# Kernel tuning notes

Measured on AMD Instinct MI355X. Metric: run time of the kernel, lower is better.

## Reference

```python
import jax, jax.numpy as jnp
import numpy as np
import math

N_HEADS = 64
N_KV_HEADS = 8
HEAD_DIM = 128
DIM = 8192
SEQLEN = 2048
KVLEN = 2048
BSZ = 1


def setup_inputs() -> dict:
    key = jax.random.key(0)
    k1, k2, k3, k4, k5 = jax.random.split(key, 5)
    xq = jax.random.normal(k1, (SEQLEN, N_HEADS, BSZ, HEAD_DIM), dtype=jnp.float32)
    keys = jax.random.normal(k2, (BSZ, N_KV_HEADS, KVLEN, HEAD_DIM), dtype=jnp.float32)
    values = jax.random.normal(k3, (BSZ, N_KV_HEADS, KVLEN, HEAD_DIM), dtype=jnp.float32)
    attn_mask = jax.random.normal(k4, (SEQLEN, 1, 1, KVLEN), dtype=jnp.float32)
    wo_w = jax.random.normal(k5, (DIM, DIM), dtype=jnp.float32) * (1.0 / math.sqrt(DIM))
    return {"xq": xq, "keys": keys, "values": values, "attn_mask": attn_mask, "wo_w": wo_w}


def reference(xq, keys, values, attn_mask, wo_w):
    n_rep = N_HEADS // N_KV_HEADS
    bsz = xq.shape[2]
    seqlen = xq.shape[0]
    # repeat_kv: expand kv heads to n_heads (torch expand+reshape == jnp.repeat on head axis)
    k = jnp.repeat(keys, n_rep, axis=1)    # (b, n_heads, kv, d)
    v = jnp.repeat(values, n_rep, axis=1)  # (b, n_heads, kv, d)
    q = jnp.transpose(xq, (2, 1, 0, 3))    # (b, n_heads, s, d)
    mask = jnp.transpose(attn_mask, (2, 1, 0, 3))  # (b_or_1, h_or_1, s, kv)
    scores = jnp.einsum('bhsd,bhtd->bhst', q, k) / math.sqrt(HEAD_DIM)
    scores = scores + mask
    probs = jax.nn.softmax(scores.astype(jnp.float32), axis=-1).astype(q.dtype)
    out = jnp.einsum('bhst,bhtd->bhsd', probs, v)  # (b, h, s, d)
    out = jnp.transpose(out, (0, 2, 1, 3)).reshape(bsz, seqlen, -1)  # (b, s, h*d)
    return out @ wo_w.T  # Linear wo, no bias
```

## Files before the change

### kernel.cpp

```cpp
#include <hip/hip_runtime.h>
#include <hip/hip_bf16.h>
#include <stdint.h>


typedef __bf16 bf16;
typedef __attribute__((ext_vector_type(8))) __bf16 bf16x8;
typedef __attribute__((ext_vector_type(4))) __bf16 bf16x4;
typedef __attribute__((ext_vector_type(4))) float f32x4;
typedef __attribute__((ext_vector_type(16))) float f32x16;
typedef __attribute__((ext_vector_type(4))) unsigned int u32x4;

#define N_HEADS 64
#define N_KVH   8
#define HDIM    128
#define SEQ     2048
#define KVL     2048
#define DIM     8192

__device__ __forceinline__ void gload16(const void* g, void* l) {
  __builtin_amdgcn_global_load_lds((const __attribute__((address_space(1))) void*)g,
                                   (__attribute__((address_space(3))) void*)l,
                                   16, 0, 0);
}

__device__ __forceinline__ unsigned pack2(float lo, float hi) {
  union { bf16 h; unsigned short u; } a, b;
  a.h = (bf16)lo; b.h = (bf16)hi;
  return ((unsigned)b.u << 16) | (unsigned)a.u;
}

__device__ __forceinline__ void exch(unsigned a, unsigned b, bool hi, unsigned& r0, unsigned& r1) {
  unsigned sa = (unsigned)__shfl_xor((int)a, 32);
  unsigned sb = (unsigned)__shfl_xor((int)b, 32);
  r0 = hi ? sb : a;
  r1 = hi ? b  : sa;
}

__device__ __forceinline__ void buildfrags(const float (&p)[16], bool hi, bf16x8& f0, bf16x8& f1) {
  unsigned pk0 = pack2(p[0],  p[1]),  pk1 = pack2(p[2],  p[3]);
  unsigned pk2 = pack2(p[4],  p[5]),  pk3 = pack2(p[6],  p[7]);
  unsigned pk4 = pack2(p[8],  p[9]),  pk5 = pack2(p[10], p[11]);
  unsigned pk6 = pack2(p[12], p[13]), pk7 = pack2(p[14], p[15]);
  unsigned a0, a1, b0, b1, c0, c1, d0, d1;
  exch(pk0, pk2, hi, a0, a1);
  exch(pk1, pk3, hi, b0, b1);
  exch(pk4, pk6, hi, c0, c1);
  exch(pk5, pk7, hi, d0, d1);
  u32x4 w0 = { a0, b0, a1, b1 };
  u32x4 w1 = { c0, d0, c1, d1 };
  f0 = __builtin_bit_cast(bf16x8, w0);
  f1 = __builtin_bit_cast(bf16x8, w1);
}

__global__ void cvt_f32_bf16(const float* __restrict__ in, bf16* __restrict__ out, int n4) {
  int i = blockIdx.x * blockDim.x + threadIdx.x;
  int stride = gridDim.x * blockDim.x;
  for (; i < n4; i += stride) {
    float4 v = ((const float4*)in)[i];
    bf16x4 o = { (bf16)v.x, (bf16)v.y, (bf16)v.z, (bf16)v.w };
    *(bf16x4*)(out + (long)i * 4) = o;
  }
}

__global__ void cvt_vT_kernel(const float* __restrict__ v, bf16* __restrict__ vT) {
  __shared__ bf16 tile[64][132];
  const int tid = threadIdx.x;
  const int kh = blockIdx.x >> 5;
  const int t0 = (blockIdx.x & 31) << 6;
  const float* src = v + ((long)kh * KVL + t0) * HDIM;
#pragma unroll
  for (int it = 0; it < 8; ++it) {
    int q = it * 256 + tid;
    int r = q >> 5;
    int c4 = (q & 31) << 2;
    float4 val = *(const float4*)(src + (long)r * HDIM + c4);
    bf16x4 o = { (bf16)val.x, (bf16)val.y, (bf16)val.z, (bf16)val.w };
    *(bf16x4*)&tile[r][c4] = o;
  }
  __syncthreads();
  const int t = tid & 63;
  const int dbase = tid >> 6;
#pragma unroll
  for (int it = 0; it < 32; ++it) {
    int d = it * 4 + dbase;
    vT[((long)kh * HDIM + d) * KVL + t0 + t] = tile[t][d];
  }
}

__global__ __launch_bounds__(512, 2) void attn_kernel(
    const bf16* __restrict__ qB, const bf16* __restrict__ kB,
    const bf16* __restrict__ vT, const float* __restrict__ mask,
    bf16* __restrict__ attnB)
{
  __shared__ __align__(16) char lds[65536];

  const int tid  = threadIdx.x;
  const int lane = tid & 63;
  const int w    = tid >> 6;
  const bool hi  = (lane >> 5) != 0;
  const int ihi  = lane >> 5;
  const int l31  = lane & 31;

  const int bid = blockIdx.x;
  const int h   = bid >> 3;
  const int q0b = (bid & 7) << 8;
  const int kh  = h >> 3;

#pragma unroll
  for (int rnd = 0; rnd < 8; ++rnd) {
    int row = rnd * 32 + w * 4 + (lane >> 4);
    int cg  = (lane & 15) ^ (row & 15);
    const bf16* g = qB + (((long)(q0b + row) * N_HEADS + h) << 7) + (cg << 3);
    gload16(g, lds + rnd * 8192 + w * 1024);
  }
  __syncthreads();

  bf16x8 qf[8];
  {
    int qrow = (w << 5) + l31;
    const char* qr = lds + qrow * 256;
#pragma unroll
    for (int s = 0; s < 8; ++s)
      qf[s] = *(const bf16x8*)(qr + ((((s << 1) | ihi) ^ (qrow & 15)) << 4));
  }
  __syncthreads();

  {
#pragma unroll
    for (int rnd = 0; rnd < 2; ++rnd) {
      int row = rnd * 32 + w * 4 + (lane >> 4);
      int cg  = (lane & 15) ^ (row & 15);
      const bf16* g = kB + (((long)(kh * KVL + row)) << 7) + (cg << 3);
      gload16(g, lds + rnd * 8192 + w * 1024);
    }
#pragma unroll
    for (int rnd = 0; rnd < 2; ++rnd) {
      int vr = rnd * 32 + w * 4 + (lane >> 4);
      int gg = (lane & 15) ^ (vr & 15);
      int dsrc = (vr << 1) | (gg >> 3);
      const bf16* gp = vT + ((long)(kh * HDIM + dsrc) * KVL) + ((gg & 7) << 3);
      gload16(gp, lds + 32768 + rnd * 8192 + w * 1024);
    }
  }
  __syncthreads();

  const float scale = 0.08838834764831845f;
  const float* mrow = mask + (size_t)(q0b + (w << 5) + l31) * KVL + (ihi << 2);

  f32x16 acc[4];
#pragma unroll
  for (int dt = 0; dt < 4; ++dt) acc[dt] = {};
  float m_run = -1e30f, l_run = 0.f;

  for (int kt = 0; kt < KVL / 64; ++kt) {
    const int cur = kt & 1;
    const int kv0 = kt << 6;

    if (kt < KVL / 64 - 1) {
      const int kv0n = kv0 + 64;
#pragma unroll
      for (int rnd = 0; rnd < 2; ++rnd) {
        int row = rnd * 32 + w * 4 + (lane >> 4);
        int cg  = (lane & 15) ^ (row & 15);
        const bf16* g = kB + (((long)(kh * KVL + kv0n + row)) << 7) + (cg << 3);
        gload16(g, lds + (cur ^ 1) * 16384 + rnd * 8192 + w * 1024);
      }
#pragma unroll
      for (int rnd = 0; rnd < 2; ++rnd) {
        int vr = rnd * 32 + w * 4 + (lane >> 4);
        int gg = (lane & 15) ^ (vr & 15);
        int dsrc = (vr << 1) | (gg >> 3);
        const bf16* gp = vT + ((long)(kh * HDIM + dsrc) * KVL) + kv0n + ((gg & 7) << 3);
        gload16(gp, lds + 32768 + (cur ^ 1) * 16384 + rnd * 8192 + w * 1024);
      }
    }

    const float* mrt = mrow + kv0;
    f32x4 mk0[4], mk1[4];
#pragma unroll
    for (int rq = 0; rq < 4; ++rq) {
      mk0[rq] = *(const f32x4*)(mrt + (rq << 3));
      mk1[rq] = *(const f32x4*)(mrt + 32 + (rq << 3));
    }

    const char* kb = lds + cur * 16384;
    f32x16 s0 = {}, s1 = {};
    const int kr0 = l31, kr1 = 32 + l31;
    __builtin_amdgcn_s_setprio(1);
#pragma unroll
    for (int s = 0; s < 8; ++s) {
      bf16x8 kf0 = *(const bf16x8*)(kb + kr0 * 256 + ((((s << 1) | ihi) ^ (kr0 & 15)) << 4));
      s0 = __builtin_amdgcn_mfma_f32_32x32x16_bf16(kf0, qf[s], s0, 0, 0, 0);
      bf16x8 kf1 = *(const bf16x8*)(kb + kr1 * 256 + ((((s << 1) | ihi) ^ (kr1 & 15)) << 4));
      s1 = __builtin_amdgcn_mfma_f32_32x32x16_bf16(kf1, qf[s], s1, 0, 0, 0);
    }
    __builtin_amdgcn_s_setprio(0);

    float p0[16], p1[16];
#pragma unroll
    for (int rq = 0; rq < 4; ++rq) {
#pragma unroll
      for (int j = 0; j < 4; ++j) {
        p0[rq * 4 + j] = s0[rq * 4 + j] * scale + mk0[rq][j];
        p1[rq * 4 + j] = s1[rq * 4 + j] * scale + mk1[rq][j];
      }
    }

    float q00 = fmaxf(fmaxf(p0[0],  p0[1]),  fmaxf(p0[2],  p0[3]));
    float q01 = fmaxf(fmaxf(p0[4],  p0[5]),  fmaxf(p0[6],  p0[7]));
    float q02 = fmaxf(fmaxf(p0[8],  p0[9]),  fmaxf(p0[10], p0[11]));
    float q03 = fmaxf(fmaxf(p0[12], p0[13]), fmaxf(p0[14], p0[15]));
    float q10 = fmaxf(fmaxf(p1[0],  p1[1]),  fmaxf(p1[2],  p1[3]));
    float q11 = fmaxf(fmaxf(p1[4],  p1[5]),  fmaxf(p1[6],  p1[7]));
    float q12 = fmaxf(fmaxf(p1[8],  p1[9]),  fmaxf(p1[10], p1[11]));
    float q13 = fmaxf(fmaxf(p1[12], p1[13]), fmaxf(p1[14], p1[15]));
    float mx = fmaxf(fmaxf(fmaxf(q00, q01), fmaxf(q02, q03)),
                     fmaxf(fmaxf(q10, q11), fmaxf(q12, q13)));
    mx = fmaxf(mx, __shfl_xor(mx, 32));
    if (!__all((int)(mx - m_run <= 8.0f))) {
      float nm = fmaxf(m_run, mx);
      float al = __expf(m_run - nm);
      m_run = nm;
      l_run *= al;
#pragma unroll
      for (int dt = 0; dt < 4; ++dt) acc[dt] *= al;
    }
    float ps = 0.f;
#pragma unroll
    for (int i = 0; i < 16; ++i) { p0[i] = __expf(p0[i] - m_run); ps += p0[i]; }
#pragma unroll
    for (int i = 0; i < 16; ++i) { p1[i] = __expf(p1[i] - m_run); ps += p1[i]; }
    ps += __shfl_xor(ps, 32);
    l_run += ps;

    bf16x8 pfrag[4];
    buildfrags(p0, hi, pfrag[0], pfrag[1]);
    buildfrags(p1, hi, pfrag[2], pfrag[3]);

    const char* vb = lds + 32768 + cur * 16384;
    const int par8 = (l31 & 1) << 3;
    __builtin_amdgcn_s_setprio(1);
#pragma unroll
    for (int dt = 0; dt < 4; ++dt) {
      const int vrow = (dt << 4) + (l31 >> 1);
      const char* vrp = vb + vrow * 256;
#pragma unroll
      for (int ks = 0; ks < 4; ++ks) {
        int c16 = par8 | (ks << 1) | ihi;
        bf16x8 vf = *(const bf16x8*)(vrp + ((c16 ^ (vrow & 15)) << 4));
        acc[dt] = __builtin_amdgcn_mfma_f32_32x32x16_bf16(vf, pfrag[ks], acc[dt], 0, 0, 0);
      }
    }
    __builtin_amdgcn_s_setprio(0);
    __syncthreads();
  }

  const float linv = 1.0f / l_run;
  char* ep = lds + (w << 13);
#pragma unroll
  for (int dt = 0; dt < 4; ++dt) {
#pragma unroll
    for (int r = 0; r < 16; ++r) {
      int d = (dt << 5) + (r & 3) + ((r >> 2) << 3) + (ihi << 2);
      int byte = l31 * 256 + (((d >> 3) ^ (l31 & 15)) << 4) + ((d & 7) << 1);
      *(bf16*)(ep + byte) = (bf16)(acc[dt][r] * linv);
    }
  }
  __syncthreads();
  const size_t obase = (size_t)(q0b + (w << 5)) * DIM + h * HDIM;
#pragma unroll
  for (int i = 0; i < 8; ++i) {
    int row = (i << 2) + (lane >> 4);
    int cp  = lane & 15;
    int c   = cp ^ (row & 15);
    bf16x8 ov = *(const bf16x8*)(ep + row * 256 + (cp << 4));
    *(bf16x8*)(attnB + obase + (size_t)row * DIM + (c << 3)) = ov;
  }
}

__global__ __launch_bounds__(512, 2) void gemm_bt(
    const bf16* __restrict__ A, const bf16* __restrict__ B, float* __restrict__ C)
{
  __shared__ __align__(16) char lds[131072];
  const int tid  = threadIdx.x;
  const int lane = tid & 63;
  const int w    = tid >> 6;
  const int wm   = w >> 2;
  const int wn   = w & 3;

  const int bid = blockIdx.x;
  const int m0  = (bid >> 5) << 8;
  const int n0  = (((bid & 7) << 2) | ((bid >> 3) & 3)) << 8;

  const int srow = tid >> 2;
  const int skey = (srow >> 1) & 3;
  const int sch  = (tid & 3) ^ skey;
  const bf16* gA0 = A + (long)(m0 + srow) * DIM + (sch << 3);
  const bf16* gA1 = gA0 + (long)128 * DIM;
  const bf16* gB0 = B + (long)(n0 + srow) * DIM + (sch << 3);
  const bf16* gB1 = gB0 + (long)128 * DIM;

  f32x4 acc[8][4];
#pragma unroll
  for (int i = 0; i < 8; ++i)
#pragma unroll
    for (int j = 0; j < 4; ++j) acc[i][j] = { 0.f, 0.f, 0.f, 0.f };

  auto STAGE = [&](int kt) {
    const long ko = (long)kt << 5;
    char* s = lds + (kt & 3) * 32768 + (w << 10);
    gload16(gA0 + ko, s);
    gload16(gA1 + ko, s + 8192);
    gload16(gB0 + ko, s + 16384);
    gload16(gB1 + ko, s + 24576);
  };

  const int g = lane >> 4;
  auto COMPUTE = [&](int slot) {
    const char* ab = lds + slot * 32768;
    const char* bb = ab + 16384;
    bf16x8 af[8], bfr[4];
#pragma unroll
    for (int i = 0; i < 8; ++i) {
      int m = (wm << 7) + (i << 4) + (lane & 15);
      af[i] = *(const bf16x8*)(ab + m * 64 + ((g ^ ((m >> 1) & 3)) << 4));
    }
#pragma unroll
    for (int j = 0; j < 4; ++j) {
      int n = (wn << 6) + (j << 4) + (lane & 15);
      bfr[j] = *(const bf16x8*)(bb + n * 64 + ((g ^ ((n >> 1) & 3)) << 4));
    }
    __builtin_amdgcn_s_setprio(1);
#pragma unroll
    for (int i = 0; i < 8; ++i)
#pragma unroll
      for (int j = 0; j < 4; ++j)
        acc[i][j] = __builtin_amdgcn_mfma_f32_16x16x32_bf16(af[i], bfr[j], acc[i][j], 0, 0, 0);
    __builtin_amdgcn_s_setprio(0);
  };

  STAGE(0);
  STAGE(1);
  STAGE(2);

#pragma unroll 4
  for (int t = 0; t < 252; ++t) {
    asm volatile("s_waitcnt vmcnt(8)" ::: "memory");
    __builtin_amdgcn_s_barrier();
    STAGE(t + 3);
    COMPUTE(t & 3);
  }
  asm volatile("s_waitcnt vmcnt(8)" ::: "memory");
  __builtin_amdgcn_s_barrier();
  STAGE(255);
  COMPUTE(0);
  asm volatile("s_waitcnt vmcnt(8)" ::: "memory");
  __builtin_amdgcn_s_barrier();
  COMPUTE(1);
  asm volatile("s_waitcnt vmcnt(4)" ::: "memory");
  __builtin_amdgcn_s_barrier();
  COMPUTE(2);
  asm volatile("s_waitcnt vmcnt(0)" ::: "memory");
  __builtin_amdgcn_s_barrier();
  COMPUTE(3);

#pragma unroll
  for (int i = 0; i < 8; ++i) {
#pragma unroll
    for (int rr = 0; rr < 4; ++rr) {
      float* cp = C + (long)(m0 + (wm << 7) + (i << 4) + ((lane >> 4) << 2) + rr) * DIM
                    + n0 + (wn << 6) + (lane & 15);
#pragma unroll
      for (int j = 0; j < 4; ++j)
        cp[j * 16] = acc[i][j][rr];
    }
  }
}

extern "C" void kernel_launch(void* const* d_in, const int* in_sizes, int n_in,
                              void* d_out, int out_size, void* d_ws, size_t ws_size,
                              hipStream_t stream) {
  const float* xq     = (const float*)d_in[0];
  const float* keys   = (const float*)d_in[1];
  const float* values = (const float*)d_in[2];
  const float* mask   = (const float*)d_in[3];
  const float* wo     = (const float*)d_in[4];
  float* out = (float*)d_out;
  char* ws = (char*)d_ws;

  bf16* woB = (bf16*)ws;
  bf16* qB  = (bf16*)(ws + 134217728ull);
  bf16* kB  = (bf16*)(ws + 134217728ull + 33554432ull);
  bf16* vT  = (bf16*)(ws + 134217728ull + 37748736ull);
  bf16* aB  = (bf16*)(ws + 134217728ull + 41943040ull);

  cvt_f32_bf16<<<dim3(2048), dim3(256), 0, stream>>>(wo, woB, 16777216);
  cvt_f32_bf16<<<dim3(1024), dim3(256), 0, stream>>>(xq, qB, 4194304);
  cvt_f32_bf16<<<dim3(256),  dim3(256), 0, stream>>>(keys, kB, 524288);
  cvt_vT_kernel<<<dim3(256), dim3(256), 0, stream>>>(values, vT);
  attn_kernel<<<dim3(512),   dim3(512), 0, stream>>>(qB, kB, vT, mask, aB);
  gemm_bt<<<dim3(256),       dim3(512), 0, stream>>>(aB, woB, out);
}
```

Before: 553.8 us.

## Software-pipeline attention loop so next QK overlaps softmax and PV

Restructures the attention main loop so the QK MFMA for tile t+1 is issued before the softmax and PV of tile t, using two score register sets and a triple-buffered V region in LDS (LDS grows to 80KB). It also folds the 1/sqrt(d) scale into the Q conversion, replaces the shuffle-based fragment exchange with v_permlane32_swap, and splits the exp-sum into four partial accumulators. The aim is to hide softmax latency behind matrix work. The cost is higher register pressure and LDS use, which may lower occupancy below two blocks per CU.

```diff
diff --git a/kernel.cpp b/kernel.cpp
--- a/kernel.cpp
+++ b/kernel.cpp
@@ -29,35 +29,35 @@
   return ((unsigned)b.u << 16) | (unsigned)a.u;
 }
 
-__device__ __forceinline__ void exch(unsigned a, unsigned b, bool hi, unsigned& r0, unsigned& r1) {
-  unsigned sa = (unsigned)__shfl_xor((int)a, 32);
-  unsigned sb = (unsigned)__shfl_xor((int)b, 32);
-  r0 = hi ? sb : a;
-  r1 = hi ? b  : sa;
-}
-
-__device__ __forceinline__ void buildfrags(const float (&p)[16], bool hi, bf16x8& f0, bf16x8& f1) {
+__device__ __forceinline__ void exch(unsigned a, unsigned b, unsigned& r0, unsigned& r1) {
+  asm("v_permlane32_swap_b32 %0, %1" : "+v"(a), "+v"(b));
+  r0 = a; r1 = b;
+}
+
+__device__ __forceinline__ void buildfrags(const float (&p)[16], bf16x8& f0, bf16x8& f1) {
   unsigned pk0 = pack2(p[0],  p[1]),  pk1 = pack2(p[2],  p[3]);
   unsigned pk2 = pack2(p[4],  p[5]),  pk3 = pack2(p[6],  p[7]);
   unsigned pk4 = pack2(p[8],  p[9]),  pk5 = pack2(p[10], p[11]);
   unsigned pk6 = pack2(p[12], p[13]), pk7 = pack2(p[14], p[15]);
   unsigned a0, a1, b0, b1, c0, c1, d0, d1;
-  exch(pk0, pk2, hi, a0, a1);
-  exch(pk1, pk3, hi, b0, b1);
-  exch(pk4, pk6, hi, c0, c1);
-  exch(pk5, pk7, hi, d0, d1);
+  exch(pk0, pk2, a0, a1);
+  exch(pk1, pk3, b0, b1);
+  exch(pk4, pk6, c0, c1);
+  exch(pk5, pk7, d0, d1);
   u32x4 w0 = { a0, b0, a1, b1 };
   u32x4 w1 = { c0, d0, c1, d1 };
   f0 = __builtin_bit_cast(bf16x8, w0);
   f1 = __builtin_bit_cast(bf16x8, w1);
 }
 
-__global__ void cvt_f32_bf16(const float* __restrict__ in, bf16* __restrict__ out, int n4) {
+__global__ void cvt_f32_bf16(const float* __restrict__ in, bf16* __restrict__ out,
+                             int n4, float scale) {
   int i = blockIdx.x * blockDim.x + threadIdx.x;
   int stride = gridDim.x * blockDim.x;
   for (; i < n4; i += stride) {
     float4 v = ((const float4*)in)[i];
-    bf16x4 o = { (bf16)v.x, (bf16)v.y, (bf16)v.z, (bf16)v.w };
+    bf16x4 o = { (bf16)(v.x * scale), (bf16)(v.y * scale),
+                 (bf16)(v.z * scale), (bf16)(v.w * scale) };
     *(bf16x4*)(out + (long)i * 4) = o;
   }
 }
@@ -87,17 +87,122 @@
   }
 }
 
+__device__ __forceinline__ void stage_kv(const bf16* __restrict__ kB,
+                                         const bf16* __restrict__ vT,
+                                         char* lds, int kh, int kvt, int w, int lane) {
+  const int kv0 = kvt << 6;
+  char* kd = lds + (kvt & 1) * 16384 + w * 1024;
+#pragma unroll
+  for (int rnd = 0; rnd < 2; ++rnd) {
+    int row = rnd * 32 + w * 4 + (lane >> 4);
+    int cg  = (lane & 15) ^ (row & 15);
+    const bf16* g = kB + (((long)(kh * KVL + kv0 + row)) << 7) + (cg << 3);
+    gload16(g, kd + rnd * 8192);
+  }
+  char* vd = lds + 32768 + (kvt % 3) * 16384 + w * 1024;
+#pragma unroll
+  for (int rnd = 0; rnd < 2; ++rnd) {
+    int vr = rnd * 32 + w * 4 + (lane >> 4);
+    int gg = (lane & 15) ^ (vr & 15);
+    int dsrc = (vr << 1) | (gg >> 3);
+    const bf16* gp = vT + ((long)(kh * HDIM + dsrc) * KVL) + kv0 + ((gg & 7) << 3);
+    gload16(gp, vd + rnd * 8192);
+  }
+}
+
+__device__ __forceinline__ void qk_cluster(const char* kb, const bf16x8 (&qf)[8],
+                                           int l31, int ihi, f32x16& s0, f32x16& s1) {
+  s0 = {}; s1 = {};
+  const int kr0 = l31, kr1 = 32 + l31;
+#pragma unroll
+  for (int s = 0; s < 8; ++s) {
+    bf16x8 kf0 = *(const bf16x8*)(kb + kr0 * 256 + ((((s << 1) | ihi) ^ (kr0 & 15)) << 4));
+    s0 = __builtin_amdgcn_mfma_f32_32x32x16_bf16(kf0, qf[s], s0, 0, 0, 0);
+    bf16x8 kf1 = *(const bf16x8*)(kb + kr1 * 256 + ((((s << 1) | ihi) ^ (kr1 & 15)) << 4));
+    s1 = __builtin_amdgcn_mfma_f32_32x32x16_bf16(kf1, qf[s], s1, 0, 0, 0);
+  }
+}
+
+__device__ __forceinline__ void softmax_step(const f32x16& s0v, const f32x16& s1v,
+    const float* mrt, float& m_run, float& l_run,
+    f32x16 (&acc)[4], bf16x8 (&pfrag)[4]) {
+  f32x4 mk0[4], mk1[4];
+#pragma unroll
+  for (int rq = 0; rq < 4; ++rq) {
+    mk0[rq] = *(const f32x4*)(mrt + (rq << 3));
+    mk1[rq] = *(const f32x4*)(mrt + 32 + (rq << 3));
+  }
+  float p0[16], p1[16];
+#pragma unroll
+  for (int rq = 0; rq < 4; ++rq)
+#pragma unroll
+    for (int j = 0; j < 4; ++j) {
+      p0[rq * 4 + j] = s0v[rq * 4 + j] + mk0[rq][j];
+      p1[rq * 4 + j] = s1v[rq * 4 + j] + mk1[rq][j];
+    }
+  float q00 = fmaxf(fmaxf(p0[0],  p0[1]),  fmaxf(p0[2],  p0[3]));
+  float q01 = fmaxf(fmaxf(p0[4],  p0[5]),  fmaxf(p0[6],  p0[7]));
+  float q02 = fmaxf(fmaxf(p0[8],  p0[9]),  fmaxf(p0[10], p0[11]));
+  float q03 = fmaxf(fmaxf(p0[12], p0[13]), fmaxf(p0[14], p0[15]));
+  float q10 = fmaxf(fmaxf(p1[0],  p1[1]),  fmaxf(p1[2],  p1[3]));
+  float q11 = fmaxf(fmaxf(p1[4],  p1[5]),  fmaxf(p1[6],  p1[7]));
+  float q12 = fmaxf(fmaxf(p1[8],  p1[9]),  fmaxf(p1[10], p1[11]));
+  float q13 = fmaxf(fmaxf(p1[12], p1[13]), fmaxf(p1[14], p1[15]));
+  float mx = fmaxf(fmaxf(fmaxf(q00, q01), fmaxf(q02, q03)),
+                   fmaxf(fmaxf(q10, q11), fmaxf(q12, q13)));
+  mx = fmaxf(mx, __shfl_xor(mx, 32));
+  if (!__all((int)(mx - m_run <= 8.0f))) {
+    float nm = fmaxf(m_run, mx);
+    float al = __expf(m_run - nm);
+    m_run = nm;
+    l_run *= al;
+#pragma unroll
+    for (int dt = 0; dt < 4; ++dt) acc[dt] *= al;
+  }
+  float ps0 = 0.f, ps1 = 0.f, ps2 = 0.f, ps3 = 0.f;
+#pragma unroll
+  for (int i = 0; i < 8; ++i) { p0[i] = __expf(p0[i] - m_run); ps0 += p0[i]; }
+#pragma unroll
+  for (int i = 8; i < 16; ++i) { p0[i] = __expf(p0[i] - m_run); ps1 += p0[i]; }
+#pragma unroll
+  for (int i = 0; i < 8; ++i) { p1[i] = __expf(p1[i] - m_run); ps2 += p1[i]; }
+#pragma unroll
+  for (int i = 8; i < 16; ++i) { p1[i] = __expf(p1[i] - m_run); ps3 += p1[i]; }
+  float ps = (ps0 + ps1) + (ps2 + ps3);
+  ps += __shfl_xor(ps, 32);
+  l_run += ps;
+  buildfrags(p0, pfrag[0], pfrag[1]);
+  buildfrags(p1, pfrag[2], pfrag[3]);
+}
+
+__device__ __forceinline__ void pv_cluster(const char* vb, const bf16x8 (&pfrag)[4],
+                                           int l31, int ihi, f32x16 (&acc)[4]) {
+  const int par8 = (l31 & 1) << 3;
+  __builtin_amdgcn_s_setprio(1);
+#pragma unroll
+  for (int dt = 0; dt < 4; ++dt) {
+    const int vrow = (dt << 4) + (l31 >> 1);
+    const char* vrp = vb + vrow * 256;
+#pragma unroll
+    for (int ks = 0; ks < 4; ++ks) {
+      int c16 = par8 | (ks << 1) | ihi;
+      bf16x8 vf = *(const bf16x8*)(vrp + ((c16 ^ (vrow & 15)) << 4));
+      acc[dt] = __builtin_amdgcn_mfma_f32_32x32x16_bf16(vf, pfrag[ks], acc[dt], 0, 0, 0);
+    }
+  }
+  __builtin_amdgcn_s_setprio(0);
+}
+
 __global__ __launch_bounds__(512, 2) void attn_kernel(
     const bf16* __restrict__ qB, const bf16* __restrict__ kB,
     const bf16* __restrict__ vT, const float* __restrict__ mask,
     bf16* __restrict__ attnB)
 {
-  __shared__ __align__(16) char lds[65536];
+  __shared__ __align__(16) char lds[81920];
 
   const int tid  = threadIdx.x;
   const int lane = tid & 63;
   const int w    = tid >> 6;
-  const bool hi  = (lane >> 5) != 0;
   const int ihi  = lane >> 5;
   const int l31  = lane & 31;
 
@@ -125,26 +230,10 @@
   }
   __syncthreads();
 
-  {
-#pragma unroll
-    for (int rnd = 0; rnd < 2; ++rnd) {
-      int row = rnd * 32 + w * 4 + (lane >> 4);
-      int cg  = (lane & 15) ^ (row & 15);
-      const bf16* g = kB + (((long)(kh * KVL + row)) << 7) + (cg << 3);
-      gload16(g, lds + rnd * 8192 + w * 1024);
-    }
-#pragma unroll
-    for (int rnd = 0; rnd < 2; ++rnd) {
-      int vr = rnd * 32 + w * 4 + (lane >> 4);
-      int gg = (lane & 15) ^ (vr & 15);
-      int dsrc = (vr << 1) | (gg >> 3);
-      const bf16* gp = vT + ((long)(kh * HDIM + dsrc) * KVL) + ((gg & 7) << 3);
-      gload16(gp, lds + 32768 + rnd * 8192 + w * 1024);
-    }
-  }
-  __syncthreads();
-
-  const float scale = 0.08838834764831845f;
+  stage_kv(kB, vT, lds, kh, 0, w, lane);
+  stage_kv(kB, vT, lds, kh, 1, w, lane);
+  __syncthreads();
+
   const float* mrow = mask + (size_t)(q0b + (w << 5) + l31) * KVL + (ihi << 2);
 
   f32x16 acc[4];
@@ -152,109 +241,33 @@
   for (int dt = 0; dt < 4; ++dt) acc[dt] = {};
   float m_run = -1e30f, l_run = 0.f;
 
-  for (int kt = 0; kt < KVL / 64; ++kt) {
-    const int cur = kt & 1;
-    const int kv0 = kt << 6;
-
-    if (kt < KVL / 64 - 1) {
-      const int kv0n = kv0 + 64;
-#pragma unroll
-      for (int rnd = 0; rnd < 2; ++rnd) {
-        int row = rnd * 32 + w * 4 + (lane >> 4);
-        int cg  = (lane & 15) ^ (row & 15);
-        const bf16* g = kB + (((long)(kh * KVL + kv0n + row)) << 7) + (cg << 3);
-        gload16(g, lds + (cur ^ 1) * 16384 + rnd * 8192 + w * 1024);
-      }
-#pragma unroll
-      for (int rnd = 0; rnd < 2; ++rnd) {
-        int vr = rnd * 32 + w * 4 + (lane >> 4);
-        int gg = (lane & 15) ^ (vr & 15);
-        int dsrc = (vr << 1) | (gg >> 3);
-        const bf16* gp = vT + ((long)(kh * HDIM + dsrc) * KVL) + kv0n + ((gg & 7) << 3);
-        gload16(gp, lds + 32768 + (cur ^ 1) * 16384 + rnd * 8192 + w * 1024);
-      }
-    }
-
-    const float* mrt = mrow + kv0;
-    f32x4 mk0[4], mk1[4];
-#pragma unroll
-    for (int rq = 0; rq < 4; ++rq) {
-      mk0[rq] = *(const f32x4*)(mrt + (rq << 3));
-      mk1[rq] = *(const f32x4*)(mrt + 32 + (rq << 3));
-    }
-
-    const char* kb = lds + cur * 16384;
-    f32x16 s0 = {}, s1 = {};
-    const int kr0 = l31, kr1 = 32 + l31;
-    __builtin_amdgcn_s_setprio(1);
-#pragma unroll
-    for (int s = 0; s < 8; ++s) {
-      bf16x8 kf0 = *(const bf16x8*)(kb + kr0 * 256 + ((((s << 1) | ihi) ^ (kr0 & 15)) << 4));
-      s0 = __builtin_amdgcn_mfma_f32_32x32x16_bf16(kf0, qf[s], s0, 0, 0, 0);
-      bf16x8 kf1 = *(const bf16x8*)(kb + kr1 * 256 + ((((s << 1) | ihi) ^ (kr1 & 15)) << 4));
-      s1 = __builtin_amdgcn_mfma_f32_32x32x16_bf16(kf1, qf[s], s1, 0, 0, 0);
-    }
-    __builtin_amdgcn_s_setprio(0);
-
-    float p0[16], p1[16];
-#pragma unroll
-    for (int rq = 0; rq < 4; ++rq) {
-#pragma unroll
-      for (int j = 0; j < 4; ++j) {
-        p0[rq * 4 + j] = s0[rq * 4 + j] * scale + mk0[rq][j];
-        p1[rq * 4 + j] = s1[rq * 4 + j] * scale + mk1[rq][j];
-      }
-    }
-
-    float q00 = fmaxf(fmaxf(p0[0],  p0[1]),  fmaxf(p0[2],  p0[3]));
-    float q01 = fmaxf(fmaxf(p0[4],  p0[5]),  fmaxf(p0[6],  p0[7]));
-    float q02 = fmaxf(fmaxf(p0[8],  p0[9]),  fmaxf(p0[10], p0[11]));
-    float q03 = fmaxf(fmaxf(p0[12], p0[13]), fmaxf(p0[14], p0[15]));
-    float q10 = fmaxf(fmaxf(p1[0],  p1[1]),  fmaxf(p1[2],  p1[3]));
-    float q11 = fmaxf(fmaxf(p1[4],  p1[5]),  fmaxf(p1[6],  p1[7]));
-    float q12 = fmaxf(fmaxf(p1[8],  p1[9]),  fmaxf(p1[10], p1[11]));
-    float q13 = fmaxf(fmaxf(p1[12], p1[13]), fmaxf(p1[14], p1[15]));
-    float mx = fmaxf(fmaxf(fmaxf(q00, q01), fmaxf(q02, q03)),
-                     fmaxf(fmaxf(q10, q11), fmaxf(q12, q13)));
-    mx = fmaxf(mx, __shfl_xor(mx, 32));
-    if (!__all((int)(mx - m_run <= 8.0f))) {
-      float nm = fmaxf(m_run, mx);
-      float al = __expf(m_run - nm);
-      m_run = nm;
-      l_run *= al;
-#pragma unroll
-      for (int dt = 0; dt < 4; ++dt) acc[dt] *= al;
-    }
-    float ps = 0.f;
-#pragma unroll
-    for (int i = 0; i < 16; ++i) { p0[i] = __expf(p0[i] - m_run); ps += p0[i]; }
-#pragma unroll
-    for (int i = 0; i < 16; ++i) { p1[i] = __expf(p1[i] - m_run); ps += p1[i]; }
-    ps += __shfl_xor(ps, 32);
-    l_run += ps;
-
-    bf16x8 pfrag[4];
-    buildfrags(p0, hi, pfrag[0], pfrag[1]);
-    buildfrags(p1, hi, pfrag[2], pfrag[3]);
-
-    const char* vb = lds + 32768 + cur * 16384;
-    const int par8 = (l31 & 1) << 3;
-    __builtin_amdgcn_s_setprio(1);
-#pragma unroll
-    for (int dt = 0; dt < 4; ++dt) {
-      const int vrow = (dt << 4) + (l31 >> 1);
-      const char* vrp = vb + vrow * 256;
-#pragma unroll
-      for (int ks = 0; ks < 4; ++ks) {
-        int c16 = par8 | (ks << 1) | ihi;
-        bf16x8 vf = *(const bf16x8*)(vrp + ((c16 ^ (vrow & 15)) << 4));
-        acc[dt] = __builtin_amdgcn_mfma_f32_32x32x16_bf16(vf, pfrag[ks], acc[dt], 0, 0, 0);
-      }
-    }
-    __builtin_amdgcn_s_setprio(0);
+  f32x16 sA0, sA1, sB0, sB1;
+  bf16x8 pfrag[4];
+
+  qk_cluster(lds, qf, l31, ihi, sA0, sA1);
+  __syncthreads();
+
+  for (int t = 1; t < 31; t += 2) {
+    stage_kv(kB, vT, lds, kh, t + 1, w, lane);
+    qk_cluster(lds + ((t & 1) * 16384), qf, l31, ihi, sB0, sB1);
+    softmax_step(sA0, sA1, mrow + ((t - 1) << 6), m_run, l_run, acc, pfrag);
+    pv_cluster(lds + 32768 + (((t - 1) % 3) * 16384), pfrag, l31, ihi, acc);
     __syncthreads();
-  }
-
+    stage_kv(kB, vT, lds, kh, t + 2, w, lane);
+    qk_cluster(lds + (((t + 1) & 1) * 16384), qf, l31, ihi, sA0, sA1);
+    softmax_step(sB0, sB1, mrow + (t << 6), m_run, l_run, acc, pfrag);
+    pv_cluster(lds + 32768 + ((t % 3) * 16384), pfrag, l31, ihi, acc);
+    __syncthreads();
+  }
+
+  qk_cluster(lds + 16384, qf, l31, ihi, sB0, sB1);
+  softmax_step(sA0, sA1, mrow + (30 << 6), m_run, l_run, acc, pfrag);
+  pv_cluster(lds + 32768 + 0 * 16384, pfrag, l31, ihi, acc);
+
+  softmax_step(sB0, sB1, mrow + (31 << 6), m_run, l_run, acc, pfrag);
+  pv_cluster(lds + 32768 + 1 * 16384, pfrag, l31, ihi, acc);
+
+  __syncthreads();
   const float linv = 1.0f / l_run;
   char* ep = lds + (w << 13);
 #pragma unroll
@@ -394,9 +407,9 @@
   bf16* vT  = (bf16*)(ws + 134217728ull + 37748736ull);
   bf16* aB  = (bf16*)(ws + 134217728ull + 41943040ull);
 
-  cvt_f32_bf16<<<dim3(2048), dim3(256), 0, stream>>>(wo, woB, 16777216);
-  cvt_f32_bf16<<<dim3(1024), dim3(256), 0, stream>>>(xq, qB, 4194304);
-  cvt_f32_bf16<<<dim3(256),  dim3(256), 0, stream>>>(keys, kB, 524288);
+  cvt_f32_bf16<<<dim3(2048), dim3(256), 0, stream>>>(wo, woB, 16777216, 1.0f);
+  cvt_f32_bf16<<<dim3(1024), dim3(256), 0, stream>>>(xq, qB, 4194304, 0.08838834764831845f);
+  cvt_f32_bf16<<<dim3(256),  dim3(256), 0, stream>>>(keys, kB, 524288, 1.0f);
   cvt_vT_kernel<<<dim3(256), dim3(256), 0, stream>>>(values, vT);
   attn_kernel<<<dim3(512),   dim3(512), 0, stream>>>(qB, kB, vT, mask, aB);
   gemm_bt<<<dim3(256),       dim3(512), 0, stream>>>(aB, woB, out);
```

Measured after the change: 560.6 us. Within noise of the previous version (+1.2%).
